# Optimization experiments

Measured on AMD Instinct MI355X. Metric: run time of the kernel, lower is better.

The kernel has to match this reference:

```python
import jax, jax.numpy as jnp
import numpy as np

H, B, N, L, V = 128, 512, 64, 64, 100000
STDV = 1.0 / float(np.sqrt(H))


def _l2norm(x):
    return x / jnp.linalg.norm(x, axis=-1, keepdims=True)


def setup_inputs() -> dict:
    key = jax.random.key(0)
    ks = list(jax.random.split(key, 24))
    u = lambda k, shape: jax.random.uniform(k, shape, dtype=jnp.float32, minval=-STDV, maxval=STDV)
    items = jax.random.randint(ks[0], (B, N), 0, V)
    A = jax.random.uniform(ks[1], (B, N, 2 * N), dtype=jnp.float32)
    alias_inputs = jax.random.randint(ks[2], (B, L), 0, N)
    # embedding is pre-normalized (torch does in-place row L2-norm on .data before use)
    emb = _l2norm(u(ks[3], (V, H)))
    return {
        "items": items, "A": A, "alias_inputs": alias_inputs,
        "emb": emb,
        "pos": u(ks[4], (L, H)),
        "linear_pos": u(ks[5], (2 * H, H)),
        "w_ih": u(ks[6], (3 * H, 2 * H)), "w_hh": u(ks[7], (3 * H, H)),
        "b_ih": u(ks[8], (3 * H,)), "b_hh": u(ks[9], (3 * H,)),
        "b_iah": u(ks[10], (H,)), "b_oah": u(ks[11], (H,)),
        "W_in": u(ks[12], (H, H)), "b_in": u(ks[13], (H,)),
        "W_out": u(ks[14], (H, H)), "b_out": u(ks[15], (H,)),
        "W1": u(ks[16], (H, H)), "b1": u(ks[17], (H,)),
        "W2": u(ks[18], (H, H)), "b2": u(ks[19], (H,)),
        "W3": u(ks[20], (1, H)),
        "Wt": u(ks[21], (H, 2 * H)), "bt": u(ks[22], (H,)),
    }


def _gnn_cell(A, hidden, W_in, b_in, W_out, b_out, b_iah, b_oah, w_ih, w_hh, b_ih, b_hh):
    n = A.shape[1]
    input_in = jnp.einsum('bnm,bmh->bnh', A[:, :, :n], hidden @ W_in.T + b_in) + b_iah
    input_out = jnp.einsum('bnm,bmh->bnh', A[:, :, n:2 * n], hidden @ W_out.T + b_out) + b_oah
    inputs = jnp.concatenate([input_in, input_out], axis=2)        # [B,N,2H]
    gi = inputs @ w_ih.T + b_ih                                     # [B,N,3H]
    gh = hidden @ w_hh.T + b_hh                                     # [B,N,3H]
    i_r, i_i, i_n = jnp.split(gi, 3, axis=2)
    h_r, h_i, h_n = jnp.split(gh, 3, axis=2)
    resetgate = jax.nn.sigmoid(i_r + h_r)
    inputgate = jax.nn.sigmoid(i_i + h_i)
    newgate = jnp.tanh(i_n + resetgate * h_n)
    return newgate + inputgate * (hidden - newgate)


def reference(items, A, alias_inputs, emb, pos, linear_pos, w_ih, w_hh, b_ih, b_hh,
              b_iah, b_oah, W_in, b_in, W_out, b_out, W1, b1, W2, b2, W3, Wt, bt):
    hidden = emb[items]                                             # [B,N,H] (dropout off in eval)
    hidden = _gnn_cell(A, hidden, W_in, b_in, W_out, b_out, b_iah, b_oah,
                       w_ih, w_hh, b_ih, b_hh)                      # step = 1
    mask = alias_inputs > 0                                         # [B,L]
    seq = jnp.take_along_axis(hidden, alias_inputs[:, :, None], axis=1)  # [B,L,H]
    pos_b = jnp.broadcast_to(pos[None, :seq.shape[1]], seq.shape)
    seq = jnp.tanh(jnp.concatenate([pos_b, seq], axis=-1) @ linear_pos)  # [B,L,H]
    seq = _l2norm(seq)
    last = jnp.sum(mask, axis=1) - 1
    ht = seq[jnp.arange(seq.shape[0]), last]                        # [B,H]
    q1 = (ht @ W1.T + b1)[:, None, :]                               # [B,1,H]
    q2 = seq @ W2.T + b2                                            # [B,L,H]
    alpha = jax.nn.sigmoid(q1 + q2) @ W3.T                          # [B,L,1]
    a = jnp.sum(alpha * seq * mask[:, :, None].astype(seq.dtype), axis=1)
    a = jnp.concatenate([a, ht], axis=1) @ Wt.T + bt                # [B,H]
    pred = 16.0 * (a @ emb[1:].T)                                   # [B,V-1], emb already L2-normed
    return pred
```

## Files before the change

kernel.cpp:

```cpp
#include <hip/hip_runtime.h>
#include <cstddef>
#include <cstdint>

#define NVOCAB 99999

typedef __attribute__((ext_vector_type(8))) short short8v;
typedef __attribute__((ext_vector_type(4))) short short4v;
typedef __attribute__((ext_vector_type(4))) float f32x4;

__device__ __forceinline__ float sigmoidf_(float x){ return 1.0f/(1.0f + __expf(-x)); }

__device__ __forceinline__ unsigned short bf16rn(float x){
    union { float f; uint32_t u; } v; v.f = x;
    uint32_t r = v.u + 0x7FFFu + ((v.u >> 16) & 1u);
    return (unsigned short)(r >> 16);
}

__device__ __forceinline__ void split_bf16(float x, unsigned short &hi, unsigned short &lo){
    hi = bf16rn(x);
    union { uint32_t u; float f; } hf; hf.u = ((uint32_t)hi) << 16;
    lo = bf16rn(x - hf.f);
}

__device__ __forceinline__ void split8(const float* xs, short8v &h, short8v &l){
    #pragma unroll
    for (int e = 0; e < 8; ++e){
        unsigned short uh, ul;
        split_bf16(xs[e], uh, ul);
        h[e] = (short)uh; l[e] = (short)ul;
    }
}

__global__ __launch_bounds__(256) void k_prep_wfrag(
    const float* __restrict__ W_in, const float* __restrict__ W_out,
    const float* __restrict__ w_ih, const float* __restrict__ w_hh,
    const float* __restrict__ lp,  const float* __restrict__ W2,
    unsigned short* __restrict__ wo_hi,
    unsigned short* __restrict__ wih_hi,
    unsigned short* __restrict__ whh_hi,
    unsigned short* __restrict__ lp_hi,  unsigned short* __restrict__ lp_lo,
    unsigned short* __restrict__ w2_hi,  unsigned short* __restrict__ w2_lo)
{
    int id = blockIdx.x*256 + threadIdx.x;
    if (id < 4096){
        int lane=id&63, tile=id>>6, nt=tile>>2, ks=tile&3;
        int col=nt*16+(lane&15), k=ks*32+(lane>>4)*8;
        const float* src = (col<128) ? (W_in + (size_t)col*128 + k) : (W_out + (size_t)(col-128)*128 + k);
        float4 f0=*(const float4*)src, f1=*(const float4*)(src+4);
        float xs[8]={f0.x,f0.y,f0.z,f0.w,f1.x,f1.y,f1.z,f1.w};
        short8v h;
        #pragma unroll
        for (int e=0;e<8;++e) h[e]=(short)bf16rn(xs[e]);
        *(short8v*)(wo_hi+(size_t)id*8)=h;
    } else if (id < 16384){
        int t2=id-4096, lane=t2&63, tile=t2>>6, nt=tile>>3, ks=tile&7;
        int col=nt*16+(lane&15), k=ks*32+(lane>>4)*8;
        const float* src = w_ih + (size_t)col*256 + k;
        float4 f0=*(const float4*)src, f1=*(const float4*)(src+4);
        short8v h;
        float xs[8]={f0.x,f0.y,f0.z,f0.w,f1.x,f1.y,f1.z,f1.w};
        #pragma unroll
        for (int e=0;e<8;++e) h[e]=(short)bf16rn(xs[e]);
        *(short8v*)(wih_hi+(size_t)t2*8)=h;
    } else if (id < 22528){
        int t3=id-16384, lane=t3&63, tile=t3>>6, nt=tile>>2, ks=tile&3;
        int col=nt*16+(lane&15), k=ks*32+(lane>>4)*8;
        const float* src = w_hh + (size_t)col*128 + k;
        float4 f0=*(const float4*)src, f1=*(const float4*)(src+4);
        short8v h;
        float xs[8]={f0.x,f0.y,f0.z,f0.w,f1.x,f1.y,f1.z,f1.w};
        #pragma unroll
        for (int e=0;e<8;++e) h[e]=(short)bf16rn(xs[e]);
        *(short8v*)(whh_hi+(size_t)t3*8)=h;
    } else if (id < 26624){
        int t4=id-22528, lane=t4&63, tile=t4>>6, nt=tile>>3, ks=tile&7;
        int col=nt*16+(lane&15), k=ks*32+(lane>>4)*8;
        float xs[8];
        #pragma unroll
        for (int e=0;e<8;++e) xs[e]=lp[(size_t)(k+e)*128 + col];
        short8v h,l; split8(xs,h,l);
        *(short8v*)(lp_hi+(size_t)t4*8)=h; *(short8v*)(lp_lo+(size_t)t4*8)=l;
    } else if (id < 28672){
        int t5=id-26624, lane=t5&63, tile=t5>>6, nt=tile>>2, ks=tile&3;
        int col=nt*16+(lane&15), k=ks*32+(lane>>4)*8;
        const float* src = W2 + (size_t)col*128 + k;
        float4 f0=*(const float4*)src, f1=*(const float4*)(src+4);
        float xs[8]={f0.x,f0.y,f0.z,f0.w,f1.x,f1.y,f1.z,f1.w};
        short8v h,l; split8(xs,h,l);
        *(short8v*)(w2_hi+(size_t)t5*8)=h; *(short8v*)(w2_lo+(size_t)t5*8)=l;
    }
}

union SharedU {
    struct { unsigned short hi[256][72]; } hvT;
    float inp[64][268];
};

__global__ __launch_bounds__(512,1) void k_gnn(
    const int* __restrict__ items, const float* __restrict__ Amat,
    const float* __restrict__ emb,
    const float* __restrict__ b_in, const float* __restrict__ b_out,
    const float* __restrict__ b_iah, const float* __restrict__ b_oah,
    const unsigned short* __restrict__ wo_hi,
    const unsigned short* __restrict__ wih_hi, const unsigned short* __restrict__ whh_hi,
    const float* __restrict__ b_ih, const float* __restrict__ b_hh,
    float* __restrict__ hidnew)
{
    const int t=threadIdx.x, lane=t&63, w=t>>6, bl=blockIdx.x;
    const int mi=w&3, ch=w>>2;
    const int c15=lane&15, g=lane>>4, kg=g*8;
    const int row=mi*16+c15;

    __shared__ int s_items[64];
    __shared__ float s_hid[64][132];
    __shared__ SharedU U;
    __shared__ unsigned short wbuf[2][24][512];

    if (t < 64) s_items[t]=items[bl*64+t];
    __syncthreads();

    {
        int r=t>>3, c0=(t&7)*16;
        const float* src = emb + (size_t)s_items[r]*128 + c0;
        float4 v0=*(const float4*)(src);
        float4 v1=*(const float4*)(src+4);
        float4 v2=*(const float4*)(src+8);
        float4 v3=*(const float4*)(src+12);
        *(float4*)&s_hid[r][c0]   = v0;
        *(float4*)&s_hid[r][c0+4] = v1;
        *(float4*)&s_hid[r][c0+8] = v2;
        *(float4*)&s_hid[r][c0+12]= v3;
    }
    __syncthreads();

    short8v hhi[4], hlo[4];
    #pragma unroll
    for (int ks=0; ks<4; ++ks){
        const float* p=&s_hid[row][ks*32+kg];
        float4 f0=*(const float4*)p, f1=*(const float4*)(p+4);
        float xs[8]={f0.x,f0.y,f0.z,f0.w,f1.x,f1.y,f1.z,f1.w};
        split8(xs,hhi[ks],hlo[ks]);
    }

    {
        f32x4 acc[8];
        #pragma unroll
        for (int nt2=0;nt2<8;++nt2){
            int col=(ch*8+nt2)*16+c15;
            float bv=(col<128)? b_in[col] : b_out[col-128];
            acc[nt2]=(f32x4){bv,bv,bv,bv};
        }
        #pragma unroll
        for (int ks=0; ks<4; ++ks){
            #pragma unroll
            for (int nt2=0; nt2<8; ++nt2){
                int nt=ch*8+nt2;
                size_t wo=((size_t)(nt*4+ks)*64+lane)*8;
                short8v bh=*(const short8v*)(wo_hi+wo);
                acc[nt2]=__builtin_amdgcn_mfma_f32_16x16x32_bf16(hhi[ks],bh,acc[nt2],0,0,0);
                acc[nt2]=__builtin_amdgcn_mfma_f32_16x16x32_bf16(hlo[ks],bh,acc[nt2],0,0,0);
            }
        }
        const int r0=g*4;
        #pragma unroll
        for (int nt2=0;nt2<8;++nt2){
            int col=(ch*8+nt2)*16+c15;
            short4v h4;
            #pragma unroll
            for (int j=0;j<4;++j) h4[j]=(short)bf16rn(acc[nt2][j]);
            *(short4v*)&U.hvT.hi[col][mi*16+r0] = h4;
        }
    }
    __syncthreads();

    f32x4 acc2[8];
    {
        #pragma unroll
        for (int nt2=0;nt2<8;++nt2){
            int col=(ch*8+nt2)*16+c15;
            float bv=(col<128)? b_iah[col] : b_oah[col-128];
            acc2[nt2]=(f32x4){bv,bv,bv,bv};
        }
        short8v ahi[2], alo[2];
        const float* Ab = Amat + (size_t)bl*8192 + (size_t)row*128 + (ch?64:0);
        #pragma unroll
        for (int ks=0;ks<2;++ks){
            float4 f0=*(const float4*)(Ab+ks*32+kg);
            float4 f1=*(const float4*)(Ab+ks*32+kg+4);
            float xs[8]={f0.x,f0.y,f0.z,f0.w,f1.x,f1.y,f1.z,f1.w};
            split8(xs,ahi[ks],alo[ks]);
        }
        #pragma unroll
        for (int ks=0;ks<2;++ks){
            #pragma unroll
            for (int nt2=0;nt2<8;++nt2){
                int h=(ch*8+nt2)*16+c15;
                int m0=ks*32+kg;
                short8v bh=*(const short8v*)&U.hvT.hi[h][m0];
                acc2[nt2]=__builtin_amdgcn_mfma_f32_16x16x32_bf16(ahi[ks],bh,acc2[nt2],0,0,0);
                acc2[nt2]=__builtin_amdgcn_mfma_f32_16x16x32_bf16(alo[ks],bh,acc2[nt2],0,0,0);
            }
        }
    }
    __syncthreads();

    {
        #pragma unroll
        for (int nt2=0;nt2<8;++nt2){
            int col=(ch*8+nt2)*16+c15;
            #pragma unroll
            for (int j=0;j<4;++j)
                U.inp[mi*16+g*4+j][col]=acc2[nt2][j];
        }
    }

    auto stage=[&](int ks, int buf){
        #pragma unroll
        for (int i=0;i<3;++i){
            int idx=i*512+t;
            int nt=idx>>6, ln=idx&63;
            const unsigned short *sh;
            if (ks<4){ sh = whh_hi + ((size_t)(nt*4+ks)*64+ln)*8; }
            else     { sh = wih_hi + ((size_t)(nt*8+(ks-4))*64+ln)*8; }
            *(short8v*)&wbuf[buf][nt][ln*8] = *(const short8v*)sh;
        }
    };

    f32x4 agi[12], agh[12];
    #pragma unroll
    for (int j=0;j<12;++j){
        int nt=(j>>2)*8 + ch*4 + (j&3);
        int col=nt*16+c15;
        float bi=b_ih[col], bh=b_hh[col];
        agi[j]=(f32x4){bi,bi,bi,bi};
        agh[j]=(f32x4){bh,bh,bh,bh};
    }

    stage(0,0);
    __syncthreads();
    for (int ks=0; ks<12; ++ks){
        int buf=ks&1;
        if (ks<11) stage(ks+1, buf^1);
        short8v ah, al;
        if (ks<4){
            ah=hhi[ks]; al=hlo[ks];
        } else {
            const float* p=&U.inp[row][(ks-4)*32+kg];
            float4 f0=*(const float4*)p, f1=*(const float4*)(p+4);
            float xs[8]={f0.x,f0.y,f0.z,f0.w,f1.x,f1.y,f1.z,f1.w};
            split8(xs,ah,al);
        }
        if (ks<4){
            #pragma unroll
            for (int j=0;j<12;++j){
                int nt=(j>>2)*8 + ch*4 + (j&3);
                short8v bh=*(const short8v*)&wbuf[buf][nt][lane*8];
                agh[j]=__builtin_amdgcn_mfma_f32_16x16x32_bf16(ah,bh,agh[j],0,0,0);
                agh[j]=__builtin_amdgcn_mfma_f32_16x16x32_bf16(al,bh,agh[j],0,0,0);
            }
        } else {
            #pragma unroll
            for (int j=0;j<12;++j){
                int nt=(j>>2)*8 + ch*4 + (j&3);
                short8v bh=*(const short8v*)&wbuf[buf][nt][lane*8];
                agi[j]=__builtin_amdgcn_mfma_f32_16x16x32_bf16(ah,bh,agi[j],0,0,0);
                agi[j]=__builtin_amdgcn_mfma_f32_16x16x32_bf16(al,bh,agi[j],0,0,0);
            }
        }
        __syncthreads();
    }

    const int r0=mi*16+g*4;
    #pragma unroll
    for (int sub=0;sub<4;++sub){
        int h=(ch*4+sub)*16+c15;
        #pragma unroll
        for (int j2=0;j2<4;++j2){
            float ir=agi[sub][j2], ii=agi[4+sub][j2], in_=agi[8+sub][j2];
            float hr=agh[sub][j2], hi_=agh[4+sub][j2], hn=agh[8+sub][j2];
            float rg=sigmoidf_(ir+hr), ig=sigmoidf_(ii+hi_);
            float ng=tanhf(in_+rg*hn);
            float ho=s_hid[r0+j2][h];
            hidnew[(size_t)(bl*64+r0+j2)*128+h]=ng+ig*(ho-ng);
        }
    }
}

__global__ __launch_bounds__(256) void k_tail(
    const int* __restrict__ alias, const float* __restrict__ pos,
    const float* __restrict__ hn,
    const unsigned short* __restrict__ lp_hi, const unsigned short* __restrict__ lp_lo,
    const unsigned short* __restrict__ w2_hi, const unsigned short* __restrict__ w2_lo,
    const float* __restrict__ b2,
    const float* __restrict__ W1, const float* __restrict__ b1,
    const float* __restrict__ W3,
    const float* __restrict__ Wt, const float* __restrict__ bt,
    unsigned short* __restrict__ pA_hi, unsigned short* __restrict__ pA_lo)
{
    const int t=threadIdx.x, lane=t&63, w=t>>6, b=blockIdx.x;
    const int c15=lane&15, g=lane>>4;

    __shared__ union { float X[64][260]; float S[64][132]; } U;
    __shared__ int s_alias[64];
    __shared__ float s_q1[128], s_ht[128], s_alpha[64], s_a[128];
    __shared__ float s_pp[2][128];
    __shared__ int s_last;

    if (t<64) s_alias[t]=alias[b*64+t];
    __syncthreads();
    if (t==0){
        int c=0;
        for (int l=0;l<64;++l) c += (s_alias[l]>0) ? 1 : 0;
        s_last=(c-1)&63;
    }
    #pragma unroll
    for (int c=0;c<8;++c){
        int flat=c*1024+t*4, l=flat>>7, k=flat&127;
        *(float4*)&U.X[l][k] = *(const float4*)(pos + l*128 + k);
        int row=s_alias[l];
        *(float4*)&U.X[l][128+k] = *(const float4*)(hn + (size_t)(b*64+row)*128 + k);
    }
    __syncthreads();

    f32x4 acc[8];
    #pragma unroll
    for (int nt=0;nt<8;++nt) acc[nt]=(f32x4){0.f,0.f,0.f,0.f};
    #pragma unroll
    for (int ks=0;ks<8;++ks){
        const float* xp=&U.X[w*16+c15][ks*32+g*8];
        float4 f0=*(const float4*)xp, f1=*(const float4*)(xp+4);
        float xs[8]={f0.x,f0.y,f0.z,f0.w,f1.x,f1.y,f1.z,f1.w};
        short8v ah,al; split8(xs,ah,al);
        #pragma unroll
        for (int nt=0;nt<8;++nt){
            size_t off=((size_t)(nt*8+ks)*64+lane)*8;
            short8v bh=*(const short8v*)(lp_hi+off);
            short8v bl_=*(const short8v*)(lp_lo+off);
            acc[nt]=__builtin_amdgcn_mfma_f32_16x16x32_bf16(ah,bh,acc[nt],0,0,0);
            acc[nt]=__builtin_amdgcn_mfma_f32_16x16x32_bf16(al,bh,acc[nt],0,0,0);
            acc[nt]=__builtin_amdgcn_mfma_f32_16x16x32_bf16(ah,bl_,acc[nt],0,0,0);
        }
    }
    float pj[4]={0.f,0.f,0.f,0.f};
    #pragma unroll
    for (int nt=0;nt<8;++nt){
        #pragma unroll
        for (int j=0;j<4;++j){
            float v=tanhf(acc[nt][j]);
            acc[nt][j]=v;
            pj[j]=fmaf(v,v,pj[j]);
        }
    }
    #pragma unroll
    for (int m=1;m<16;m<<=1){
        #pragma unroll
        for (int j=0;j<4;++j) pj[j]+=__shfl_xor(pj[j],m,64);
    }
    float rn[4];
    #pragma unroll
    for (int j=0;j<4;++j) rn[j]=rsqrtf(pj[j]);

    __syncthreads();
    #pragma unroll
    for (int nt=0;nt<8;++nt){
        #pragma unroll
        for (int j=0;j<4;++j)
            U.S[w*16+g*4+j][nt*16+c15]=acc[nt][j]*rn[j];
    }
    __syncthreads();

    if (t<128) s_ht[t]=U.S[s_last][t];
    __syncthreads();

    {
        int h=t&127, half=t>>7;
        float o=0.f;
        const float* wr=W1+(size_t)h*128+half*64;
        const float* hp=s_ht+half*64;
        #pragma unroll 8
        for (int k=0;k<64;k+=4){
            float4 wv=*(const float4*)(wr+k);
            o += hp[k]*wv.x + hp[k+1]*wv.y + hp[k+2]*wv.z + hp[k+3]*wv.w;
        }
        s_pp[half][h]=o;
    }
    __syncthreads();
    if (t<128) s_q1[t]=b1[t]+s_pp[0][t]+s_pp[1][t];

    f32x4 acc2[8];
    #pragma unroll
    for (int nt=0;nt<8;++nt){
        float bv=b2[nt*16+c15];
        acc2[nt]=(f32x4){bv,bv,bv,bv};
    }
    #pragma unroll
    for (int ks=0;ks<4;++ks){
        const float* sp=&U.S[w*16+c15][ks*32+g*8];
        float4 f0=*(const float4*)sp, f1=*(const float4*)(sp+4);
        float xs[8]={f0.x,f0.y,f0.z,f0.w,f1.x,f1.y,f1.z,f1.w};
        short8v ah,al; split8(xs,ah,al);
        #pragma unroll
        for (int nt=0;nt<8;++nt){
            size_t off=((size_t)(nt*4+ks)*64+lane)*8;
            short8v bh=*(const short8v*)(w2_hi+off);
            short8v bl_=*(const short8v*)(w2_lo+off);
            acc2[nt]=__builtin_amdgcn_mfma_f32_16x16x32_bf16(ah,bh,acc2[nt],0,0,0);
            acc2[nt]=__builtin_amdgcn_mfma_f32_16x16x32_bf16(al,bh,acc2[nt],0,0,0);
            acc2[nt]=__builtin_amdgcn_mfma_f32_16x16x32_bf16(ah,bl_,acc2[nt],0,0,0);
        }
    }
    __syncthreads();

    {
        float pa[4]={0.f,0.f,0.f,0.f};
        #pragma unroll
        for (int nt=0;nt<8;++nt){
            int col=nt*16+c15;
            float w3v=W3[col];
            #pragma unroll
            for (int j=0;j<4;++j)
                pa[j]=fmaf(sigmoidf_(s_q1[col]+acc2[nt][j]), w3v, pa[j]);
        }
        #pragma unroll
        for (int m=1;m<16;m<<=1){
            #pragma unroll
            for (int j=0;j<4;++j) pa[j]+=__shfl_xor(pa[j],m,64);
        }
        if (c15==0){
            #pragma unroll
            for (int j=0;j<4;++j){
                int l=w*16+g*4+j;
                s_alpha[l]=(s_alias[l]>0)? pa[j] : 0.f;
            }
        }
    }
    __syncthreads();

    {
        int h=t&127, half=t>>7;
        float a_=0.f;
        #pragma unroll 8
        for (int l=half*32;l<half*32+32;++l) a_=fmaf(s_alpha[l],U.S[l][h],a_);
        s_pp[half][h]=a_;
    }
    __syncthreads();
    if (t<128) s_a[t]=s_pp[0][t]+s_pp[1][t];
    __syncthreads();

    {
        int h=t&127, half=t>>7;
        float o=0.f;
        const float* wr=Wt+(size_t)h*256+half*128;
        const float* vp=(half==0)? s_a : s_ht;
        #pragma unroll 8
        for (int k=0;k<128;k+=4){
            float4 wv=*(const float4*)(wr+k);
            o += vp[k]*wv.x + vp[k+1]*wv.y + vp[k+2]*wv.z + vp[k+3]*wv.w;
        }
        s_pp[half][h]=o;
    }
    __syncthreads();
    if (t<128){
        float o=bt[t]+s_pp[0][t]+s_pp[1][t];
        unsigned short hi,lo; split_bf16(o,hi,lo);
        int mt=b>>4, r15=b&15;
        int ks=t>>5, gg=(t>>3)&3, e=t&7;
        int lz=gg*16+r15;
        size_t off=(((size_t)mt*4+ks)*64+lz)*8+e;
        pA_hi[off]=hi; pA_lo[off]=lo;
    }
}

__global__ __launch_bounds__(512,1) void k_pred_mfma(
    const unsigned short* __restrict__ Ahi, const unsigned short* __restrict__ Alo,
    const float* __restrict__ emb, float* __restrict__ outp)
{
    const int t=threadIdx.x, lane=t&63, w=t>>6;
    const int st=blockIdx.x;
    const int c15=lane&15, g=lane>>4;

    __shared__ unsigned short Bsh[32768];
    __shared__ float S[8][8][264];

    #pragma unroll
    for (int p=0;p<16;++p){
        int c = p*512 + t;
        int r = c>>5, k0 = (c&31)*4;
        int v = st*256 + r;
        int srcr = (v < NVOCAB) ? (v+1) : 0;
        float4 f = *(const float4*)(emb + (size_t)srcr*128 + k0);
        int q_s = (r>>6)*16 + ((r>>4)&3)*4 + (k0>>5);
        int ln  = ((k0>>3)&3)*16 + (r&15);
        short4v h4;
        h4[0]=(short)bf16rn(f.x); h4[1]=(short)bf16rn(f.y);
        h4[2]=(short)bf16rn(f.z); h4[3]=(short)bf16rn(f.w);
        *(short4v*)&Bsh[(q_s*64+ln)*8 + (k0&7)] = h4;
    }
    __syncthreads();

    for (int rg=0; rg<4; ++rg){
        const int mt = rg*8 + w;
        short8v ahi[4], alo[4];
        #pragma unroll
        for (int ks=0;ks<4;++ks){
            size_t off=((size_t)(mt*4+ks)*64+lane)*8;
            ahi[ks]=*(const short8v*)(Ahi+off);
            alo[ks]=*(const short8v*)(Alo+off);
        }

        f32x4 acc[16];
        __builtin_amdgcn_s_setprio(1);
        #pragma unroll
        for (int ntl=0;ntl<16;++ntl){
            acc[ntl]=(f32x4){0.f,0.f,0.f,0.f};
            #pragma unroll
            for (int ks=0;ks<4;++ks){
                short8v bh = *(const short8v*)&Bsh[(size_t)((ntl*4+ks)*64 + lane)*8];
                acc[ntl]=__builtin_amdgcn_mfma_f32_16x16x32_bf16(ahi[ks],bh,acc[ntl],0,0,0);
                acc[ntl]=__builtin_amdgcn_mfma_f32_16x16x32_bf16(alo[ks],bh,acc[ntl],0,0,0);
            }
        }
        __builtin_amdgcn_s_setprio(0);

        #pragma unroll
        for (int hh=0; hh<2; ++hh){
            if ((g>>1) == hh){
                int rloc=(g&1)*4;
                #pragma unroll
                for (int ntl=0;ntl<16;++ntl){
                    #pragma unroll
                    for (int j=0;j<4;++j)
                        S[w][rloc+j][ntl*16+c15] = 16.0f*acc[ntl][j];
                }
            }
            __syncthreads();
            #pragma unroll
            for (int p=0;p<8;++p){
                int row = mt*16 + hh*8 + p;
                int col0 = st*256 + lane*4;
                f32x4 o = *(f32x4*)&S[w][p][lane*4];
                size_t rowoff = (size_t)row*NVOCAB;
                if (col0 + 3 < NVOCAB){
                    __builtin_nontemporal_store(o, (f32x4*)(outp + rowoff + col0));
                } else {
                    #pragma unroll
                    for (int cc2=0;cc2<4;++cc2)
                        if (col0+cc2 < NVOCAB) outp[rowoff + col0 + cc2] = o[cc2];
                }
            }
            __syncthreads();
        }
    }
}

extern "C" void kernel_launch(void* const* d_in, const int* in_sizes, int n_in,
                              void* d_out, int out_size, void* d_ws, size_t ws_size,
                              hipStream_t stream)
{
    const int*   items = (const int*)  d_in[0];
    const float* Amat  = (const float*)d_in[1];
    const int*   alias = (const int*)  d_in[2];
    const float* emb   = (const float*)d_in[3];
    const float* pos   = (const float*)d_in[4];
    const float* lp    = (const float*)d_in[5];
    const float* w_ih  = (const float*)d_in[6];
    const float* w_hh  = (const float*)d_in[7];
    const float* b_ih  = (const float*)d_in[8];
    const float* b_hh  = (const float*)d_in[9];
    const float* b_iah = (const float*)d_in[10];
    const float* b_oah = (const float*)d_in[11];
    const float* W_in  = (const float*)d_in[12];
    const float* b_in  = (const float*)d_in[13];
    const float* W_out = (const float*)d_in[14];
    const float* b_out = (const float*)d_in[15];
    const float* W1    = (const float*)d_in[16];
    const float* b1    = (const float*)d_in[17];
    const float* W2    = (const float*)d_in[18];
    const float* b2    = (const float*)d_in[19];
    const float* W3    = (const float*)d_in[20];
    const float* Wt    = (const float*)d_in[21];
    const float* bt    = (const float*)d_in[22];
    float* outp = (float*)d_out;

    float* wsf = (float*)d_ws;
    size_t o = 0;
    float* hidnew = wsf + o;               o += 4194304;
    unsigned short* us = (unsigned short*)(wsf + o);
    size_t uo = 0;
    unsigned short* wo_hi  = us + uo; uo += 32768;
    unsigned short* wih_hi = us + uo; uo += 98304;
    unsigned short* whh_hi = us + uo; uo += 49152;
    unsigned short* lp_hi  = us + uo; uo += 32768;
    unsigned short* lp_lo  = us + uo; uo += 32768;
    unsigned short* w2_hi  = us + uo; uo += 16384;
    unsigned short* w2_lo  = us + uo; uo += 16384;
    unsigned short* pA_hi  = us + uo; uo += 65536;
    unsigned short* pA_lo  = us + uo; uo += 65536;

    k_prep_wfrag<<<112, 256, 0, stream>>>(W_in, W_out, w_ih, w_hh, lp, W2,
                                          wo_hi, wih_hi, whh_hi,
                                          lp_hi, lp_lo, w2_hi, w2_lo);
    k_gnn<<<512, 512, 0, stream>>>(items, Amat, emb, b_in, b_out, b_iah, b_oah,
                                   wo_hi, wih_hi, whh_hi, b_ih, b_hh, hidnew);
    k_tail<<<512, 256, 0, stream>>>(alias, pos, hidnew,
                                    lp_hi, lp_lo, w2_hi, w2_lo, b2,
                                    W1, b1, W3, Wt, bt, pA_hi, pA_lo);
    k_pred_mfma<<<391, 512, 0, stream>>>(pA_hi, pA_lo, emb, outp);
}
```

Baseline: 168.7 us.

## Fuse GNN cell and attention tail into one kernel, keeping hidden state in LDS

Merges k_gnn and k_tail into a single kernel per batch row. The GRU output now stays in shared memory instead of round-tripping through a 16 MB global buffer, and one kernel launch is removed. The pos matrix is pre-split into bf16 hi/lo MFMA fragments in the prep kernel, and the tail work is redistributed across 512 threads with an LDS union. The cost is higher LDS pressure in an already large kernel and some idle threads in the GEMV phases.

```diff
diff --git a/kernel.cpp b/kernel.cpp
--- a/kernel.cpp
+++ b/kernel.cpp
@@ -35,11 +35,13 @@
     const float* __restrict__ W_in, const float* __restrict__ W_out,
     const float* __restrict__ w_ih, const float* __restrict__ w_hh,
     const float* __restrict__ lp,  const float* __restrict__ W2,
+    const float* __restrict__ pos,
     unsigned short* __restrict__ wo_hi,
     unsigned short* __restrict__ wih_hi,
     unsigned short* __restrict__ whh_hi,
     unsigned short* __restrict__ lp_hi,  unsigned short* __restrict__ lp_lo,
-    unsigned short* __restrict__ w2_hi,  unsigned short* __restrict__ w2_lo)
+    unsigned short* __restrict__ w2_hi,  unsigned short* __restrict__ w2_lo,
+    unsigned short* __restrict__ posf_hi, unsigned short* __restrict__ posf_lo)
 {
     int id = blockIdx.x*256 + threadIdx.x;
     if (id < 4096){
@@ -88,6 +90,14 @@
         float xs[8]={f0.x,f0.y,f0.z,f0.w,f1.x,f1.y,f1.z,f1.w};
         short8v h,l; split8(xs,h,l);
         *(short8v*)(w2_hi+(size_t)t5*8)=h; *(short8v*)(w2_lo+(size_t)t5*8)=l;
+    } else if (id < 29696){
+        int t6=id-28672, lane=t6&63, tile=t6>>6, mi=tile>>2, ks=tile&3;
+        int row=mi*16+(lane&15), k=ks*32+(lane>>4)*8;
+        const float* src = pos + (size_t)row*128 + k;
+        float4 f0=*(const float4*)src, f1=*(const float4*)(src+4);
+        float xs[8]={f0.x,f0.y,f0.z,f0.w,f1.x,f1.y,f1.z,f1.w};
+        short8v h,l; split8(xs,h,l);
+        *(short8v*)(posf_hi+(size_t)t6*8)=h; *(short8v*)(posf_lo+(size_t)t6*8)=l;
     }
 }
 
@@ -96,28 +106,44 @@
     float inp[64][268];
 };
 
-__global__ __launch_bounds__(512,1) void k_gnn(
+__global__ __launch_bounds__(512,1) void k_gnn_tail(
     const int* __restrict__ items, const float* __restrict__ Amat,
-    const float* __restrict__ emb,
+    const float* __restrict__ emb, const int* __restrict__ alias,
     const float* __restrict__ b_in, const float* __restrict__ b_out,
     const float* __restrict__ b_iah, const float* __restrict__ b_oah,
     const unsigned short* __restrict__ wo_hi,
     const unsigned short* __restrict__ wih_hi, const unsigned short* __restrict__ whh_hi,
     const float* __restrict__ b_ih, const float* __restrict__ b_hh,
-    float* __restrict__ hidnew)
+    const unsigned short* __restrict__ posf_hi, const unsigned short* __restrict__ posf_lo,
+    const unsigned short* __restrict__ lp_hi, const unsigned short* __restrict__ lp_lo,
+    const unsigned short* __restrict__ w2_hi, const unsigned short* __restrict__ w2_lo,
+    const float* __restrict__ b2,
+    const float* __restrict__ W1, const float* __restrict__ b1,
+    const float* __restrict__ W3,
+    const float* __restrict__ Wt, const float* __restrict__ bt,
+    unsigned short* __restrict__ pA_hi, unsigned short* __restrict__ pA_lo)
 {
     const int t=threadIdx.x, lane=t&63, w=t>>6, bl=blockIdx.x;
     const int mi=w&3, ch=w>>2;
     const int c15=lane&15, g=lane>>4, kg=g*8;
     const int row=mi*16+c15;
 
-    __shared__ int s_items[64];
+    __shared__ int s_items[64], s_alias[64];
+    __shared__ int s_last;
     __shared__ float s_hid[64][132];
-    __shared__ SharedU U;
-    __shared__ unsigned short wbuf[2][24][512];
-
-    if (t < 64) s_items[t]=items[bl*64+t];
-    __syncthreads();
+    __shared__ union {
+        struct { SharedU U; unsigned short wbuf[2][24][512]; } gn;
+        struct { float S[64][132]; float pp2[2][128]; float alpha[64];
+                 float a[128]; float pp4[4][128]; } tl;
+    } V;
+
+    if (t < 64){ s_items[t]=items[bl*64+t]; s_alias[t]=alias[bl*64+t]; }
+    __syncthreads();
+    if (t == 0){
+        int c=0;
+        for (int l=0;l<64;++l) c += (s_alias[l]>0) ? 1 : 0;
+        s_last=(c-1)&63;
+    }
 
     {
         int r=t>>3, c0=(t&7)*16;
@@ -168,7 +194,7 @@
             short4v h4;
             #pragma unroll
             for (int j=0;j<4;++j) h4[j]=(short)bf16rn(acc[nt2][j]);
-            *(short4v*)&U.hvT.hi[col][mi*16+r0] = h4;
+            *(short4v*)&V.gn.U.hvT.hi[col][mi*16+r0] = h4;
         }
     }
     __syncthreads();
@@ -196,7 +222,7 @@
             for (int nt2=0;nt2<8;++nt2){
                 int h=(ch*8+nt2)*16+c15;
                 int m0=ks*32+kg;
-                short8v bh=*(const short8v*)&U.hvT.hi[h][m0];
+                short8v bh=*(const short8v*)&V.gn.U.hvT.hi[h][m0];
                 acc2[nt2]=__builtin_amdgcn_mfma_f32_16x16x32_bf16(ahi[ks],bh,acc2[nt2],0,0,0);
                 acc2[nt2]=__builtin_amdgcn_mfma_f32_16x16x32_bf16(alo[ks],bh,acc2[nt2],0,0,0);
             }
@@ -210,7 +236,7 @@
             int col=(ch*8+nt2)*16+c15;
             #pragma unroll
             for (int j=0;j<4;++j)
-                U.inp[mi*16+g*4+j][col]=acc2[nt2][j];
+                V.gn.U.inp[mi*16+g*4+j][col]=acc2[nt2][j];
         }
     }
 
@@ -222,7 +248,7 @@
             const unsigned short *sh;
             if (ks<4){ sh = whh_hi + ((size_t)(nt*4+ks)*64+ln)*8; }
             else     { sh = wih_hi + ((size_t)(nt*8+(ks-4))*64+ln)*8; }
-            *(short8v*)&wbuf[buf][nt][ln*8] = *(const short8v*)sh;
+            *(short8v*)&V.gn.wbuf[buf][nt][ln*8] = *(const short8v*)sh;
         }
     };
 
@@ -245,7 +271,7 @@
         if (ks<4){
             ah=hhi[ks]; al=hlo[ks];
         } else {
-            const float* p=&U.inp[row][(ks-4)*32+kg];
+            const float* p=&V.gn.U.inp[row][(ks-4)*32+kg];
             float4 f0=*(const float4*)p, f1=*(const float4*)(p+4);
             float xs[8]={f0.x,f0.y,f0.z,f0.w,f1.x,f1.y,f1.z,f1.w};
             split8(xs,ah,al);
@@ -254,7 +280,7 @@
             #pragma unroll
             for (int j=0;j<12;++j){
                 int nt=(j>>2)*8 + ch*4 + (j&3);
-                short8v bh=*(const short8v*)&wbuf[buf][nt][lane*8];
+                short8v bh=*(const short8v*)&V.gn.wbuf[buf][nt][lane*8];
                 agh[j]=__builtin_amdgcn_mfma_f32_16x16x32_bf16(ah,bh,agh[j],0,0,0);
                 agh[j]=__builtin_amdgcn_mfma_f32_16x16x32_bf16(al,bh,agh[j],0,0,0);
             }
@@ -262,7 +288,7 @@
             #pragma unroll
             for (int j=0;j<12;++j){
                 int nt=(j>>2)*8 + ch*4 + (j&3);
-                short8v bh=*(const short8v*)&wbuf[buf][nt][lane*8];
+                short8v bh=*(const short8v*)&V.gn.wbuf[buf][nt][lane*8];
                 agi[j]=__builtin_amdgcn_mfma_f32_16x16x32_bf16(ah,bh,agi[j],0,0,0);
                 agi[j]=__builtin_amdgcn_mfma_f32_16x16x32_bf16(al,bh,agi[j],0,0,0);
             }
@@ -270,143 +296,131 @@
         __syncthreads();
     }
 
-    const int r0=mi*16+g*4;
-    #pragma unroll
-    for (int sub=0;sub<4;++sub){
-        int h=(ch*4+sub)*16+c15;
-        #pragma unroll
-        for (int j2=0;j2<4;++j2){
-            float ir=agi[sub][j2], ii=agi[4+sub][j2], in_=agi[8+sub][j2];
-            float hr=agh[sub][j2], hi_=agh[4+sub][j2], hn=agh[8+sub][j2];
-            float rg=sigmoidf_(ir+hr), ig=sigmoidf_(ii+hi_);
-            float ng=tanhf(in_+rg*hn);
-            float ho=s_hid[r0+j2][h];
-            hidnew[(size_t)(bl*64+r0+j2)*128+h]=ng+ig*(ho-ng);
-        }
-    }
-}
-
-__global__ __launch_bounds__(256) void k_tail(
-    const int* __restrict__ alias, const float* __restrict__ pos,
-    const float* __restrict__ hn,
-    const unsigned short* __restrict__ lp_hi, const unsigned short* __restrict__ lp_lo,
-    const unsigned short* __restrict__ w2_hi, const unsigned short* __restrict__ w2_lo,
-    const float* __restrict__ b2,
-    const float* __restrict__ W1, const float* __restrict__ b1,
-    const float* __restrict__ W3,
-    const float* __restrict__ Wt, const float* __restrict__ bt,
-    unsigned short* __restrict__ pA_hi, unsigned short* __restrict__ pA_lo)
-{
-    const int t=threadIdx.x, lane=t&63, w=t>>6, b=blockIdx.x;
-    const int c15=lane&15, g=lane>>4;
-
-    __shared__ union { float X[64][260]; float S[64][132]; } U;
-    __shared__ int s_alias[64];
-    __shared__ float s_q1[128], s_ht[128], s_alpha[64], s_a[128];
-    __shared__ float s_pp[2][128];
-    __shared__ int s_last;
-
-    if (t<64) s_alias[t]=alias[b*64+t];
-    __syncthreads();
-    if (t==0){
-        int c=0;
-        for (int l=0;l<64;++l) c += (s_alias[l]>0) ? 1 : 0;
-        s_last=(c-1)&63;
-    }
-    #pragma unroll
-    for (int c=0;c<8;++c){
-        int flat=c*1024+t*4, l=flat>>7, k=flat&127;
-        *(float4*)&U.X[l][k] = *(const float4*)(pos + l*128 + k);
-        int row=s_alias[l];
-        *(float4*)&U.X[l][128+k] = *(const float4*)(hn + (size_t)(b*64+row)*128 + k);
-    }
-    __syncthreads();
-
-    f32x4 acc[8];
-    #pragma unroll
-    for (int nt=0;nt<8;++nt) acc[nt]=(f32x4){0.f,0.f,0.f,0.f};
-    #pragma unroll
-    for (int ks=0;ks<8;++ks){
-        const float* xp=&U.X[w*16+c15][ks*32+g*8];
-        float4 f0=*(const float4*)xp, f1=*(const float4*)(xp+4);
-        float xs[8]={f0.x,f0.y,f0.z,f0.w,f1.x,f1.y,f1.z,f1.w};
-        short8v ah,al; split8(xs,ah,al);
-        #pragma unroll
-        for (int nt=0;nt<8;++nt){
-            size_t off=((size_t)(nt*8+ks)*64+lane)*8;
-            short8v bh=*(const short8v*)(lp_hi+off);
-            short8v bl_=*(const short8v*)(lp_lo+off);
-            acc[nt]=__builtin_amdgcn_mfma_f32_16x16x32_bf16(ah,bh,acc[nt],0,0,0);
-            acc[nt]=__builtin_amdgcn_mfma_f32_16x16x32_bf16(al,bh,acc[nt],0,0,0);
-            acc[nt]=__builtin_amdgcn_mfma_f32_16x16x32_bf16(ah,bl_,acc[nt],0,0,0);
-        }
-    }
-    float pj[4]={0.f,0.f,0.f,0.f};
-    #pragma unroll
-    for (int nt=0;nt<8;++nt){
+    {
+        const int r0=mi*16+g*4;
+        #pragma unroll
+        for (int sub=0;sub<4;++sub){
+            int h=(ch*4+sub)*16+c15;
+            #pragma unroll
+            for (int j2=0;j2<4;++j2){
+                float ir=agi[sub][j2], ii=agi[4+sub][j2], in_=agi[8+sub][j2];
+                float hr=agh[sub][j2], hi_=agh[4+sub][j2], hn=agh[8+sub][j2];
+                float rg=sigmoidf_(ir+hr), ig=sigmoidf_(ii+hi_);
+                float ng=tanhf(in_+rg*hn);
+                float ho=s_hid[r0+j2][h];
+                s_hid[r0+j2][h]=ng+ig*(ho-ng);
+            }
+        }
+    }
+    __syncthreads();
+
+    {
+        const int arow = s_alias[row];
+        short8v yhi[8], ylo[8];
+        #pragma unroll
+        for (int ks=0;ks<4;++ks){
+            size_t off=((size_t)(mi*4+ks)*64+lane)*8;
+            yhi[ks]=*(const short8v*)(posf_hi+off);
+            ylo[ks]=*(const short8v*)(posf_lo+off);
+        }
+        #pragma unroll
+        for (int ks=0;ks<4;++ks){
+            const float* p=&s_hid[arow][ks*32+kg];
+            float4 f0=*(const float4*)p, f1=*(const float4*)(p+4);
+            float xs[8]={f0.x,f0.y,f0.z,f0.w,f1.x,f1.y,f1.z,f1.w};
+            split8(xs,yhi[4+ks],ylo[4+ks]);
+        }
+        f32x4 yac[4];
+        #pragma unroll
+        for (int nt2=0;nt2<4;++nt2) yac[nt2]=(f32x4){0.f,0.f,0.f,0.f};
+        #pragma unroll
+        for (int ks=0;ks<8;++ks){
+            #pragma unroll
+            for (int nt2=0;nt2<4;++nt2){
+                int nt=ch*4+nt2;
+                size_t off=((size_t)(nt*8+ks)*64+lane)*8;
+                short8v bh=*(const short8v*)(lp_hi+off);
+                short8v bl_=*(const short8v*)(lp_lo+off);
+                yac[nt2]=__builtin_amdgcn_mfma_f32_16x16x32_bf16(yhi[ks],bh,yac[nt2],0,0,0);
+                yac[nt2]=__builtin_amdgcn_mfma_f32_16x16x32_bf16(ylo[ks],bh,yac[nt2],0,0,0);
+                yac[nt2]=__builtin_amdgcn_mfma_f32_16x16x32_bf16(yhi[ks],bl_,yac[nt2],0,0,0);
+            }
+        }
+        float pj[4]={0.f,0.f,0.f,0.f};
+        #pragma unroll
+        for (int nt2=0;nt2<4;++nt2){
+            #pragma unroll
+            for (int j=0;j<4;++j){
+                float v=tanhf(yac[nt2][j]);
+                yac[nt2][j]=v;
+                pj[j]=fmaf(v,v,pj[j]);
+            }
+        }
+        #pragma unroll
+        for (int m=1;m<16;m<<=1){
+            #pragma unroll
+            for (int j=0;j<4;++j) pj[j]+=__shfl_xor(pj[j],m,64);
+        }
+        if (c15==0){
+            #pragma unroll
+            for (int j=0;j<4;++j) V.tl.pp2[ch][mi*16+g*4+j]=pj[j];
+        }
+        __syncthreads();
+        float rn[4];
         #pragma unroll
         for (int j=0;j<4;++j){
-            float v=tanhf(acc[nt][j]);
-            acc[nt][j]=v;
-            pj[j]=fmaf(v,v,pj[j]);
-        }
-    }
-    #pragma unroll
-    for (int m=1;m<16;m<<=1){
-        #pragma unroll
-        for (int j=0;j<4;++j) pj[j]+=__shfl_xor(pj[j],m,64);
-    }
-    float rn[4];
-    #pragma unroll
-    for (int j=0;j<4;++j) rn[j]=rsqrtf(pj[j]);
-
-    __syncthreads();
-    #pragma unroll
-    for (int nt=0;nt<8;++nt){
-        #pragma unroll
-        for (int j=0;j<4;++j)
-            U.S[w*16+g*4+j][nt*16+c15]=acc[nt][j]*rn[j];
-    }
-    __syncthreads();
-
-    if (t<128) s_ht[t]=U.S[s_last][t];
-    __syncthreads();
-
-    {
-        int h=t&127, half=t>>7;
-        float o=0.f;
-        const float* wr=W1+(size_t)h*128+half*64;
-        const float* hp=s_ht+half*64;
-        #pragma unroll 8
-        for (int k=0;k<64;k+=4){
-            float4 wv=*(const float4*)(wr+k);
-            o += hp[k]*wv.x + hp[k+1]*wv.y + hp[k+2]*wv.z + hp[k+3]*wv.w;
-        }
-        s_pp[half][h]=o;
-    }
-    __syncthreads();
-    if (t<128) s_q1[t]=b1[t]+s_pp[0][t]+s_pp[1][t];
-
-    f32x4 acc2[8];
-    #pragma unroll
-    for (int nt=0;nt<8;++nt){
-        float bv=b2[nt*16+c15];
-        acc2[nt]=(f32x4){bv,bv,bv,bv};
-    }
-    #pragma unroll
-    for (int ks=0;ks<4;++ks){
-        const float* sp=&U.S[w*16+c15][ks*32+g*8];
-        float4 f0=*(const float4*)sp, f1=*(const float4*)(sp+4);
-        float xs[8]={f0.x,f0.y,f0.z,f0.w,f1.x,f1.y,f1.z,f1.w};
-        short8v ah,al; split8(xs,ah,al);
-        #pragma unroll
-        for (int nt=0;nt<8;++nt){
-            size_t off=((size_t)(nt*4+ks)*64+lane)*8;
-            short8v bh=*(const short8v*)(w2_hi+off);
-            short8v bl_=*(const short8v*)(w2_lo+off);
-            acc2[nt]=__builtin_amdgcn_mfma_f32_16x16x32_bf16(ah,bh,acc2[nt],0,0,0);
-            acc2[nt]=__builtin_amdgcn_mfma_f32_16x16x32_bf16(al,bh,acc2[nt],0,0,0);
-            acc2[nt]=__builtin_amdgcn_mfma_f32_16x16x32_bf16(ah,bl_,acc2[nt],0,0,0);
+            int r=mi*16+g*4+j;
+            rn[j]=rsqrtf(V.tl.pp2[0][r]+V.tl.pp2[1][r]);
+        }
+        #pragma unroll
+        for (int nt2=0;nt2<4;++nt2){
+            #pragma unroll
+            for (int j=0;j<4;++j)
+                V.tl.S[mi*16+g*4+j][(ch*4+nt2)*16+c15]=yac[nt2][j]*rn[j];
+        }
+    }
+    __syncthreads();
+
+    f32x4 qac[4];
+    {
+        if (t < 256){
+            int h=t&127, half=t>>7;
+            float o=0.f;
+            const float* wr=W1+(size_t)h*128+half*64;
+            #pragma unroll 8
+            for (int k=0;k<64;k+=4){
+                float4 wv=*(const float4*)(wr+k);
+                int kk=half*64+k;
+                o += V.tl.S[s_last][kk]*wv.x + V.tl.S[s_last][kk+1]*wv.y
+                   + V.tl.S[s_last][kk+2]*wv.z + V.tl.S[s_last][kk+3]*wv.w;
+            }
+            V.tl.pp4[half][h]=o;
+        }
+        #pragma unroll
+        for (int nt2=0;nt2<4;++nt2){
+            float bv=b2[(ch*4+nt2)*16+c15];
+            qac[nt2]=(f32x4){bv,bv,bv,bv};
+        }
+        short8v shi[4], slo[4];
+        #pragma unroll
+        for (int ks=0;ks<4;++ks){
+            const float* p=&V.tl.S[row][ks*32+kg];
+            float4 f0=*(const float4*)p, f1=*(const float4*)(p+4);
+            float xs[8]={f0.x,f0.y,f0.z,f0.w,f1.x,f1.y,f1.z,f1.w};
+            split8(xs,shi[ks],slo[ks]);
+        }
+        #pragma unroll
+        for (int ks=0;ks<4;++ks){
+            #pragma unroll
+            for (int nt2=0;nt2<4;++nt2){
+                int nt=ch*4+nt2;
+                size_t off=((size_t)(nt*4+ks)*64+lane)*8;
+                short8v bh=*(const short8v*)(w2_hi+off);
+                short8v bl_=*(const short8v*)(w2_lo+off);
+                qac[nt2]=__builtin_amdgcn_mfma_f32_16x16x32_bf16(shi[ks],bh,qac[nt2],0,0,0);
+                qac[nt2]=__builtin_amdgcn_mfma_f32_16x16x32_bf16(slo[ks],bh,qac[nt2],0,0,0);
+                qac[nt2]=__builtin_amdgcn_mfma_f32_16x16x32_bf16(shi[ks],bl_,qac[nt2],0,0,0);
+            }
         }
     }
     __syncthreads();
@@ -414,12 +428,13 @@
     {
         float pa[4]={0.f,0.f,0.f,0.f};
         #pragma unroll
-        for (int nt=0;nt<8;++nt){
-            int col=nt*16+c15;
+        for (int nt2=0;nt2<4;++nt2){
+            int col=(ch*4+nt2)*16+c15;
+            float q1c=b1[col]+V.tl.pp4[0][col]+V.tl.pp4[1][col];
             float w3v=W3[col];
             #pragma unroll
             for (int j=0;j<4;++j)
-                pa[j]=fmaf(sigmoidf_(s_q1[col]+acc2[nt][j]), w3v, pa[j]);
+                pa[j]=fmaf(sigmoidf_(q1c+qac[nt2][j]), w3v, pa[j]);
         }
         #pragma unroll
         for (int m=1;m<16;m<<=1){
@@ -428,42 +443,43 @@
         }
         if (c15==0){
             #pragma unroll
-            for (int j=0;j<4;++j){
-                int l=w*16+g*4+j;
-                s_alpha[l]=(s_alias[l]>0)? pa[j] : 0.f;
-            }
-        }
-    }
-    __syncthreads();
-
-    {
-        int h=t&127, half=t>>7;
+            for (int j=0;j<4;++j) V.tl.pp2[ch][mi*16+g*4+j]=pa[j];
+        }
+    }
+    __syncthreads();
+    if (t<64) V.tl.alpha[t]=(s_alias[t]>0)? (V.tl.pp2[0][t]+V.tl.pp2[1][t]) : 0.f;
+    __syncthreads();
+
+    {
+        int h=t&127, q4=t>>7;
         float a_=0.f;
-        #pragma unroll 8
-        for (int l=half*32;l<half*32+32;++l) a_=fmaf(s_alpha[l],U.S[l][h],a_);
-        s_pp[half][h]=a_;
-    }
-    __syncthreads();
-    if (t<128) s_a[t]=s_pp[0][t]+s_pp[1][t];
-    __syncthreads();
-
-    {
+        #pragma unroll 4
+        for (int l=q4*16;l<q4*16+16;++l) a_=fmaf(V.tl.alpha[l],V.tl.S[l][h],a_);
+        V.tl.pp4[q4][h]=a_;
+    }
+    __syncthreads();
+    if (t<128) V.tl.a[t]=V.tl.pp4[0][t]+V.tl.pp4[1][t]+V.tl.pp4[2][t]+V.tl.pp4[3][t];
+    __syncthreads();
+
+    if (t < 256){
         int h=t&127, half=t>>7;
         float o=0.f;
         const float* wr=Wt+(size_t)h*256+half*128;
-        const float* vp=(half==0)? s_a : s_ht;
         #pragma unroll 8
         for (int k=0;k<128;k+=4){
             float4 wv=*(const float4*)(wr+k);
-            o += vp[k]*wv.x + vp[k+1]*wv.y + vp[k+2]*wv.z + vp[k+3]*wv.w;
-        }
-        s_pp[half][h]=o;
+            float v0,v1,v2,v3;
+            if (half==0){ v0=V.tl.a[k]; v1=V.tl.a[k+1]; v2=V.tl.a[k+2]; v3=V.tl.a[k+3]; }
+            else        { v0=V.tl.S[s_last][k]; v1=V.tl.S[s_last][k+1]; v2=V.tl.S[s_last][k+2]; v3=V.tl.S[s_last][k+3]; }
+            o += v0*wv.x + v1*wv.y + v2*wv.z + v3*wv.w;
+        }
+        V.tl.pp2[half][h]=o;
     }
     __syncthreads();
     if (t<128){
-        float o=bt[t]+s_pp[0][t]+s_pp[1][t];
+        float o=bt[t]+V.tl.pp2[0][t]+V.tl.pp2[1][t];
         unsigned short hi,lo; split_bf16(o,hi,lo);
-        int mt=b>>4, r15=b&15;
+        int mt=bl>>4, r15=bl&15;
         int ks=t>>5, gg=(t>>3)&3, e=t&7;
         int lz=gg*16+r15;
         size_t off=(((size_t)mt*4+ks)*64+lz)*8+e;
@@ -582,28 +598,28 @@
     const float* bt    = (const float*)d_in[22];
     float* outp = (float*)d_out;
 
-    float* wsf = (float*)d_ws;
-    size_t o = 0;
-    float* hidnew = wsf + o;               o += 4194304;
-    unsigned short* us = (unsigned short*)(wsf + o);
+    unsigned short* us = (unsigned short*)d_ws;
     size_t uo = 0;
-    unsigned short* wo_hi  = us + uo; uo += 32768;
-    unsigned short* wih_hi = us + uo; uo += 98304;
-    unsigned short* whh_hi = us + uo; uo += 49152;
-    unsigned short* lp_hi  = us + uo; uo += 32768;
-    unsigned short* lp_lo  = us + uo; uo += 32768;
-    unsigned short* w2_hi  = us + uo; uo += 16384;
-    unsigned short* w2_lo  = us + uo; uo += 16384;
-    unsigned short* pA_hi  = us + uo; uo += 65536;
-    unsigned short* pA_lo  = us + uo; uo += 65536;
-
-    k_prep_wfrag<<<112, 256, 0, stream>>>(W_in, W_out, w_ih, w_hh, lp, W2,
+    unsigned short* wo_hi   = us + uo; uo += 32768;
+    unsigned short* wih_hi  = us + uo; uo += 98304;
+    unsigned short* whh_hi  = us + uo; uo += 49152;
+    unsigned short* lp_hi   = us + uo; uo += 32768;
+    unsigned short* lp_lo   = us + uo; uo += 32768;
+    unsigned short* w2_hi   = us + uo; uo += 16384;
+    unsigned short* w2_lo   = us + uo; uo += 16384;
+    unsigned short* posf_hi = us + uo; uo += 8192;
+    unsigned short* posf_lo = us + uo; uo += 8192;
+    unsigned short* pA_hi   = us + uo; uo += 65536;
+    unsigned short* pA_lo   = us + uo; uo += 65536;
+
+    k_prep_wfrag<<<116, 256, 0, stream>>>(W_in, W_out, w_ih, w_hh, lp, W2, pos,
                                           wo_hi, wih_hi, whh_hi,
-                                          lp_hi, lp_lo, w2_hi, w2_lo);
-    k_gnn<<<512, 512, 0, stream>>>(items, Amat, emb, b_in, b_out, b_iah, b_oah,
-                                   wo_hi, wih_hi, whh_hi, b_ih, b_hh, hidnew);
-    k_tail<<<512, 256, 0, stream>>>(alias, pos, hidnew,
-                                    lp_hi, lp_lo, w2_hi, w2_lo, b2,
-                                    W1, b1, W3, Wt, bt, pA_hi, pA_lo);
+                                          lp_hi, lp_lo, w2_hi, w2_lo,
+                                          posf_hi, posf_lo);
+    k_gnn_tail<<<512, 512, 0, stream>>>(items, Amat, emb, alias,
+                                        b_in, b_out, b_iah, b_oah,
+                                        wo_hi, wih_hi, whh_hi, b_ih, b_hh,
+                                        posf_hi, posf_lo, lp_hi, lp_lo, w2_hi, w2_lo, b2,
+                                        W1, b1, W3, Wt, bt, pA_hi, pA_lo);
     k_pred_mfma<<<391, 512, 0, stream>>>(pA_hi, pA_lo, emb, outp);
 }
```

New measurement: 176.9 us. +4.8%, slower.
